# Kernel tuning notes

Measured on AMD Instinct MI355X. Metric: run time of the kernel, lower is better.

Reference implementation:

```python
import jax, jax.numpy as jnp
import numpy as np

N_ENSEMBLE = 50
STATE_DIM = 32
ACTION_DIM = 8
HIDDEN = 256
BATCH = 8192
OUT_DIM = STATE_DIM + 1  # next_state + reward


def setup_inputs() -> dict:
    key = jax.random.key(0)
    ks = jax.random.split(key, 8)
    s = 0.05  # small init scale to keep activations sane
    return {
        "state": jax.random.normal(ks[0], (BATCH, STATE_DIM), dtype=jnp.float32),
        "action": jax.random.normal(ks[1], (BATCH, ACTION_DIM), dtype=jnp.float32),
        "W1": jax.random.normal(ks[2], (N_ENSEMBLE, STATE_DIM + ACTION_DIM, HIDDEN), dtype=jnp.float32) * s,
        "b1": jnp.zeros((N_ENSEMBLE, HIDDEN), dtype=jnp.float32),
        "W2": jax.random.normal(ks[3], (N_ENSEMBLE, HIDDEN, HIDDEN), dtype=jnp.float32) * s,
        "b2": jnp.zeros((N_ENSEMBLE, HIDDEN), dtype=jnp.float32),
        "W3": jax.random.normal(ks[4], (N_ENSEMBLE, HIDDEN, HIDDEN), dtype=jnp.float32) * s,
        "b3": jnp.zeros((N_ENSEMBLE, HIDDEN), dtype=jnp.float32),
        "W4": jax.random.normal(ks[5], (N_ENSEMBLE, HIDDEN, OUT_DIM), dtype=jnp.float32) * s,
        "b4": jnp.zeros((N_ENSEMBLE, OUT_DIM), dtype=jnp.float32),
    }


def reference(state, action, W1, b1, W2, b2, W3, b3, W4, b4):
    # state_action: [B, S+A] shared across all ensemble members
    sa = jnp.concatenate((state, action), axis=1)
    # Batched-over-ensemble GEMMs replace the python loop over 50 MLPs.
    # h: [B, E, H]
    h = jax.nn.relu(jnp.einsum("bi,eih->beh", sa, W1) + b1)
    h = jax.nn.relu(jnp.einsum("beh,ehk->bek", h, W2) + b2)
    h = jax.nn.relu(jnp.einsum("beh,ehk->bek", h, W3) + b3)
    preds = jnp.einsum("beh,eho->beo", h, W4) + b4  # [B, E, S+1]
    return preds[..., :-1], preds[..., -1]
```

## Files before the change

### kernel.cpp

```cpp
#include <hip/hip_runtime.h>


typedef __attribute__((ext_vector_type(8))) short short8;
typedef __attribute__((ext_vector_type(4))) float floatx4;

#define NE 50
#define NB 8192
#define OUT_NS_ELEMS (NB * NE * 32)
#define OSTRIDE 48

__device__ __forceinline__ unsigned short f2bf_rne(float x) {
  unsigned u = __float_as_uint(x);
  u += 0x7fffu + ((u >> 16) & 1u);
  return (unsigned short)(u >> 16);
}
__device__ __forceinline__ float bf2f(unsigned short b) {
  return __uint_as_float(((unsigned)b) << 16);
}
__device__ __forceinline__ floatx4 mfma16(short8 a, short8 b, floatx4 c) {
  return __builtin_amdgcn_mfma_f32_16x16x32_bf16(a, b, c, 0, 0, 0);
}
__device__ __forceinline__ unsigned pack_bf2(float lo, float hi) {
  unsigned u0 = __float_as_uint(lo) + 0x8000u;
  unsigned u1 = __float_as_uint(hi) + 0x8000u;
  return __builtin_amdgcn_perm(u1, u0, 0x07060302u);
}

__device__ __forceinline__ unsigned short load_bf(const void* p, long i, bool isbf) {
  if (isbf) return ((const unsigned short*)p)[i];
  return f2bf_rne(((const float*)p)[i]);
}
__device__ __forceinline__ float load_f(const void* p, long i, bool isbf) {
  if (isbf) return bf2f(((const unsigned short*)p)[i]);
  return ((const float*)p)[i];
}

__device__ void pack_w_panel(const void* __restrict__ src, unsigned short* __restrict__ dst,
                             bool isbf, int e, int kt, int K, int N, int NT, int perE,
                             unsigned short* lds) {
  const int t = threadIdx.x;
  const int Npad = NT * 16;
  const int NP = Npad + 10;
  if (!isbf && N == Npad) {
    const int nq = Npad >> 2;
    for (int idx = t; idx < 32 * nq; idx += 256) {
      int r = idx / nq, q = idx - r * nq;
      int k = kt * 32 + r;
      unsigned short v0 = 0, v1 = 0, v2 = 0, v3 = 0;
      if (k < K) {
        const float4 f =
            *(const float4*)((const float*)src + ((long)(e * K + k) * N + q * 4));
        v0 = f2bf_rne(f.x); v1 = f2bf_rne(f.y);
        v2 = f2bf_rne(f.z); v3 = f2bf_rne(f.w);
      }
      unsigned* p = (unsigned*)(lds + r * NP + q * 4);
      p[0] = (unsigned)v0 | ((unsigned)v1 << 16);
      p[1] = (unsigned)v2 | ((unsigned)v3 << 16);
    }
  } else if (isbf && N == Npad) {
    const int no = Npad >> 3;
    for (int idx = t; idx < 32 * no; idx += 256) {
      int r = idx / no, q = idx - r * no;
      int k = kt * 32 + r;
      uint4 f = make_uint4(0u, 0u, 0u, 0u);
      if (k < K)
        f = *(const uint4*)((const unsigned short*)src + ((long)(e * K + k) * N + q * 8));
      unsigned* p = (unsigned*)(lds + r * NP + q * 8);
      p[0] = f.x; p[1] = f.y; p[2] = f.z; p[3] = f.w;
    }
  } else {
    for (int idx = t; idx < 32 * Npad; idx += 256) {
      int r = idx / Npad, c = idx - r * Npad;
      int k = kt * 32 + r;
      unsigned short v = 0;
      if (k < K && c < N) v = load_bf(src, (long)(e * K + k) * N + c, isbf);
      lds[r * NP + c] = v;
    }
  }
  __syncthreads();
  for (int u = t; u < NT * 64; u += 256) {
    int nt = u >> 6, kb = (u >> 4) & 3, ni = u & 15;
    int n = nt * 16 + ni;
    unsigned v[4];
#pragma unroll
    for (int p = 0; p < 4; ++p) {
      unsigned lo = lds[(kb * 8 + 2 * p) * NP + n];
      unsigned hi = lds[(kb * 8 + 2 * p + 1) * NP + n];
      v[p] = lo | (hi << 16);
    }
    long off = (long)e * perE + ((long)((kt * NT + nt) * 64 + kb * 16 + ni)) * 8;
    *(uint4*)(dst + off) = make_uint4(v[0], v[1], v[2], v[3]);
  }
}

__global__ void k_pack(const void* __restrict__ state, const void* __restrict__ action,
                       const void* __restrict__ W1, const void* __restrict__ W2,
                       const void* __restrict__ W3, const void* __restrict__ W4,
                       const void* __restrict__ b1, const void* __restrict__ b2,
                       const void* __restrict__ b3, const void* __restrict__ b4,
                       int isbfi,
                       unsigned short* __restrict__ saP, unsigned short* __restrict__ w1P,
                       unsigned short* __restrict__ w2P, unsigned short* __restrict__ w3P,
                       unsigned short* __restrict__ w4P, float* __restrict__ biasP) {
  __shared__ unsigned short lds[32 * 266];
  const bool isbf = (isbfi != 0);
  const int b = blockIdx.x;
  if (b < 400) {
    pack_w_panel(W2, w2P, isbf, b >> 3, b & 7, 256, 256, 16, 65536, lds);
  } else if (b < 800) {
    int bb = b - 400;
    pack_w_panel(W3, w3P, isbf, bb >> 3, bb & 7, 256, 256, 16, 65536, lds);
  } else if (b < 900) {
    int bb = b - 800;
    pack_w_panel(W1, w1P, isbf, bb >> 1, bb & 1, 40, 256, 16, 16384, lds);
  } else if (b < 1300) {
    int bb = b - 900;
    pack_w_panel(W4, w4P, isbf, bb >> 3, bb & 7, 256, 33, 3, 12288, lds);
  } else if (b < 1556) {
    int u = (b - 1300) * 256 + threadIdx.x;
    int mi = u & 15, kb = (u >> 4) & 7, mt = u >> 7;
    int row = mt * 16 + mi;
    unsigned v[4] = {0u, 0u, 0u, 0u};
    if (kb < 4) {
#pragma unroll
      for (int p = 0; p < 4; ++p) {
        unsigned lo = load_bf(state, (long)row * 32 + kb * 8 + 2 * p, isbf);
        unsigned hi = load_bf(state, (long)row * 32 + kb * 8 + 2 * p + 1, isbf);
        v[p] = lo | (hi << 16);
      }
    } else if (kb == 4) {
#pragma unroll
      for (int p = 0; p < 4; ++p) {
        unsigned lo = load_bf(action, (long)row * 8 + 2 * p, isbf);
        unsigned hi = load_bf(action, (long)row * 8 + 2 * p + 1, isbf);
        v[p] = lo | (hi << 16);
      }
    }
    *(uint4*)(saP + (long)u * 8) = make_uint4(v[0], v[1], v[2], v[3]);
  } else {
    int gid = (b - 1556) * 256 + threadIdx.x;
    if (gid < NE * 816) {
      int e = gid / 816, r = gid - e * 816;
      float v = 0.0f;
      if (r < 256)      v = load_f(b1, e * 256 + r,         isbf);
      else if (r < 512) v = load_f(b2, e * 256 + (r - 256), isbf);
      else if (r < 768) v = load_f(b3, e * 256 + (r - 512), isbf);
      else { int q = r - 768; if (q < 33) v = load_f(b4, e * 33 + q, isbf); }
      biasP[gid] = v;
    }
  }
}


__device__ __forceinline__ void store_tile16(const floatx4& a4, unsigned short* hT,
                                             int FT, int BT, int li, int g) {
  int k0 = FT * 16 + g * 4;
  unsigned d0 = pack_bf2(fmaxf(a4[0], 0.0f), fmaxf(a4[1], 0.0f));
  unsigned d1 = pack_bf2(fmaxf(a4[2], 0.0f), fmaxf(a4[3], 0.0f));
  int addr = ((k0 >> 5) * 4 + BT) * 512 + ((k0 >> 3) & 3) * 128 + li * 8 + (k0 & 7);
  *(unsigned long long*)(hT + addr) =
      (unsigned long long)d0 | ((unsigned long long)d1 << 32);
}

__device__ __forceinline__ void hidden_layer(const unsigned short* __restrict__ wp,
                                             const float* __restrict__ br,
                                             unsigned short* hT,
                                             int wf, int l, int li, int g) {
  floatx4 acc[4][4];
#pragma unroll
  for (int ot = 0; ot < 4; ++ot) {
    const float4 bq = *(const float4*)(br + wf * 64 + ot * 16 + g * 4);
    floatx4 iv = {bq.x, bq.y, bq.z, bq.w};
#pragma unroll
    for (int bt = 0; bt < 4; ++bt) acc[ot][bt] = iv;
  }
#pragma unroll
  for (int kt = 0; kt < 8; ++kt) {
    short8 a[4];
#pragma unroll
    for (int ot = 0; ot < 4; ++ot)
      a[ot] = *(const short8*)(wp + (long)((kt * 16 + wf * 4 + ot) * 64 + l) * 8);
#pragma unroll
    for (int bt = 0; bt < 4; ++bt) {
      short8 b = *(const short8*)(hT + ((kt * 4 + bt) * 64 + l) * 8);
#pragma unroll
      for (int ot = 0; ot < 4; ++ot)
        acc[ot][bt] = mfma16(a[ot], b, acc[ot][bt]);
    }
  }
  __syncthreads();
#pragma unroll
  for (int ot = 0; ot < 4; ++ot)
#pragma unroll
    for (int bt = 0; bt < 4; ++bt)
      store_tile16(acc[ot][bt], hT, wf * 4 + ot, bt, li, g);
  __syncthreads();
}

__global__ __launch_bounds__(256, 4) void k_mlp(
    const unsigned short* __restrict__ sa,
    const unsigned short* __restrict__ w1,
    const unsigned short* __restrict__ w2,
    const unsigned short* __restrict__ w3,
    const unsigned short* __restrict__ w4,
    const float* __restrict__ bias,
    int isbfi,
    float* __restrict__ rewardWS,
    void* __restrict__ outp) {
  __shared__ __attribute__((aligned(16))) unsigned short hT[16384];
  const int tid = threadIdx.x;
  const int wf = tid >> 6, l = tid & 63, li = l & 15, g = l >> 4;

  const int lid = blockIdx.y * 128 + blockIdx.x;
  const int swz = (lid & 7) * 800 + (lid >> 3);
  const int e  = swz >> 7;
  const int bb = swz & 127;

  const float* brow = bias + e * 816;
  const bool isbf = (isbfi != 0);

  {
    floatx4 acc[4][4];
#pragma unroll
    for (int ot = 0; ot < 4; ++ot) {
      const float4 bq = *(const float4*)(brow + wf * 64 + ot * 16 + g * 4);
      floatx4 iv = {bq.x, bq.y, bq.z, bq.w};
#pragma unroll
      for (int bt = 0; bt < 4; ++bt) acc[ot][bt] = iv;
    }
#pragma unroll
    for (int kt = 0; kt < 2; ++kt) {
      short8 a[4];
#pragma unroll
      for (int ot = 0; ot < 4; ++ot)
        a[ot] = *(const short8*)(w1 + (long)e * 16384 +
                                 (long)((kt * 16 + wf * 4 + ot) * 64 + l) * 8);
#pragma unroll
      for (int bt = 0; bt < 4; ++bt) {
        short8 b = *(const short8*)(sa + (long)((bb * 4 + bt) * 128 + kt * 64 + l) * 8);
#pragma unroll
        for (int ot = 0; ot < 4; ++ot)
          acc[ot][bt] = mfma16(a[ot], b, acc[ot][bt]);
      }
    }
#pragma unroll
    for (int ot = 0; ot < 4; ++ot)
#pragma unroll
      for (int bt = 0; bt < 4; ++bt)
        store_tile16(acc[ot][bt], hT, wf * 4 + ot, bt, li, g);
    __syncthreads();
  }

  hidden_layer(w2 + (long)e * 65536, brow + 256, hT, wf, l, li, g);
  hidden_layer(w3 + (long)e * 65536, brow + 512, hT, wf, l, li, g);

  const float* brow4 = brow + 768;
  floatx4 acc4[3];
#pragma unroll
  for (int ft = 0; ft < 3; ++ft) {
    const float4 bq = *(const float4*)(brow4 + ft * 16 + g * 4);
    floatx4 iv = {bq.x, bq.y, bq.z, bq.w};
    acc4[ft] = iv;
  }
#pragma unroll
  for (int kt = 0; kt < 8; ++kt) {
    short8 a[3];
#pragma unroll
    for (int ft = 0; ft < 3; ++ft)
      a[ft] = *(const short8*)(w4 + (long)e * 12288 + (long)((kt * 3 + ft) * 64 + l) * 8);
    short8 b = *(const short8*)(hT + ((kt * 4 + wf) * 64 + l) * 8);
#pragma unroll
    for (int ft = 0; ft < 3; ++ft)
      acc4[ft] = mfma16(a[ft], b, acc4[ft]);
  }

  if (g == 0) {
    rewardWS[(long)e * NB + bb * 64 + wf * 16 + li] = acc4[2][0];
  }

  __syncthreads();
#pragma unroll
  for (int ft = 0; ft < 2; ++ft) {
    int batch = wf * 16 + li;
    unsigned d0 = pack_bf2(acc4[ft][0], acc4[ft][1]);
    unsigned d1 = pack_bf2(acc4[ft][2], acc4[ft][3]);
    *(unsigned long long*)(hT + batch * OSTRIDE + ft * 16 + g * 4) =
        (unsigned long long)d0 | ((unsigned long long)d1 << 32);
  }
  __syncthreads();

  if (isbf) {
    unsigned short* o16 = (unsigned short*)outp;
    int batch = tid >> 2;
    int chunk = tid & 3;
    uint4 v = *(const uint4*)(hT + batch * OSTRIDE + chunk * 8);
    *(uint4*)(o16 + ((long)(bb * 64 + batch) * NE + e) * 32 + chunk * 8) = v;
  } else {
    float* o32 = (float*)outp;
#pragma unroll
    for (int p = 0; p < 2; ++p) {
      int idx = p * 256 + tid;
      int batch = idx >> 3;
      int chunk = idx & 7;
      const unsigned short* s = hT + batch * OSTRIDE + chunk * 4;
      *(float4*)(o32 + ((long)(bb * 64 + batch) * NE + e) * 32 + chunk * 4) =
          make_float4(bf2f(s[0]), bf2f(s[1]), bf2f(s[2]), bf2f(s[3]));
    }
  }
}

__global__ void k_reward(const float* __restrict__ rw, int isbfi,
                         void* __restrict__ outp) {
  int id = blockIdx.x * 256 + threadIdx.x;
  if (id >= NB * NE) return;
  int b = id / NE, e = id - b * NE;
  float v = rw[(long)e * NB + b];
  if (isbfi != 0) {
    unsigned u = __float_as_uint(v) + 0x8000u;
    ((unsigned short*)outp)[OUT_NS_ELEMS + id] = (unsigned short)(u >> 16);
  } else {
    ((float*)outp)[OUT_NS_ELEMS + id] = v;
  }
}

extern "C" void kernel_launch(void* const* d_in, const int* in_sizes, int n_in,
                              void* d_out, int out_size, void* d_ws, size_t ws_size,
                              hipStream_t stream) {
  const void* state  = d_in[0];
  const void* action = d_in[1];
  const void* W1 = d_in[2];
  const void* b1 = d_in[3];
  const void* W2 = d_in[4];
  const void* b2 = d_in[5];
  const void* W3 = d_in[6];
  const void* b3 = d_in[7];
  const void* W4 = d_in[8];
  const void* b4 = d_in[9];
  (void)n_in; (void)out_size; (void)ws_size;

  const int isbf = (in_sizes[4] == NE * 256 * 256 * 2) ? 1 : 0;

  char* ws = (char*)d_ws;
  unsigned short* saP    = (unsigned short*)(ws + 256);
  unsigned short* w1P    = (unsigned short*)(ws + 1048832);
  unsigned short* w2P    = (unsigned short*)(ws + 2687232);
  unsigned short* w3P    = (unsigned short*)(ws + 9240832);
  unsigned short* w4P    = (unsigned short*)(ws + 15794432);
  float* biasP           = (float*)(ws + 17023232);
  float* rewardWS        = (float*)(ws + 17186432);

  k_pack<<<1716, 256, 0, stream>>>(state, action, W1, W2, W3, W4, b1, b2, b3, b4,
                                   isbf, saP, w1P, w2P, w3P, w4P, biasP);
  k_mlp<<<dim3(128, 50), 256, 0, stream>>>(saP, w1P, w2P, w3P, w4P, biasP, isbf,
                                           rewardWS, d_out);
  k_reward<<<(NB * NE + 255) / 256, 256, 0, stream>>>(rewardWS, isbf, d_out);
}
```

Before: 236.3 us.

## Split weight packing into half-panels, vectorize input packing, add MFMA priority hints

Weight-panel packing now handles 16 K-rows per block instead of 32, which doubles the pack grid and halves the LDS staging buffer. This should raise occupancy and parallelism in the pack kernel. State/action packing now uses vectorized float4/uint4 loads, with each block handling four chunks instead of scalar loads. The MLP kernel wraps its MFMA inner loops in s_setprio(1)/s_setprio(0) so matrix issue gets priority over other waves. The extra blocks add launch overhead, and the setprio hints may have little effect.

```diff
diff --git a/kernel.cpp b/kernel.cpp
--- a/kernel.cpp
+++ b/kernel.cpp
@@ -35,17 +35,18 @@
   return ((const float*)p)[i];
 }
 
-__device__ void pack_w_panel(const void* __restrict__ src, unsigned short* __restrict__ dst,
-                             bool isbf, int e, int kt, int K, int N, int NT, int perE,
-                             unsigned short* lds) {
+__device__ void pack_w_panel16(const void* __restrict__ src, unsigned short* __restrict__ dst,
+                               bool isbf, int e, int kt, int h, int K, int N, int NT,
+                               int perE, unsigned short* lds) {
   const int t = threadIdx.x;
   const int Npad = NT * 16;
   const int NP = Npad + 10;
+  const int k0 = kt * 32 + h * 16;
   if (!isbf && N == Npad) {
     const int nq = Npad >> 2;
-    for (int idx = t; idx < 32 * nq; idx += 256) {
+    for (int idx = t; idx < 16 * nq; idx += 256) {
       int r = idx / nq, q = idx - r * nq;
-      int k = kt * 32 + r;
+      int k = k0 + r;
       unsigned short v0 = 0, v1 = 0, v2 = 0, v3 = 0;
       if (k < K) {
         const float4 f =
@@ -59,9 +60,9 @@
     }
   } else if (isbf && N == Npad) {
     const int no = Npad >> 3;
-    for (int idx = t; idx < 32 * no; idx += 256) {
+    for (int idx = t; idx < 16 * no; idx += 256) {
       int r = idx / no, q = idx - r * no;
-      int k = kt * 32 + r;
+      int k = k0 + r;
       uint4 f = make_uint4(0u, 0u, 0u, 0u);
       if (k < K)
         f = *(const uint4*)((const unsigned short*)src + ((long)(e * K + k) * N + q * 8));
@@ -69,23 +70,24 @@
       p[0] = f.x; p[1] = f.y; p[2] = f.z; p[3] = f.w;
     }
   } else {
-    for (int idx = t; idx < 32 * Npad; idx += 256) {
+    for (int idx = t; idx < 16 * Npad; idx += 256) {
       int r = idx / Npad, c = idx - r * Npad;
-      int k = kt * 32 + r;
+      int k = k0 + r;
       unsigned short v = 0;
       if (k < K && c < N) v = load_bf(src, (long)(e * K + k) * N + c, isbf);
       lds[r * NP + c] = v;
     }
   }
   __syncthreads();
-  for (int u = t; u < NT * 64; u += 256) {
-    int nt = u >> 6, kb = (u >> 4) & 3, ni = u & 15;
+  for (int u = t; u < NT * 32; u += 256) {
+    int ni = u & 15, kb_loc = (u >> 4) & 1, nt = u >> 5;
     int n = nt * 16 + ni;
+    int kb = 2 * h + kb_loc;
     unsigned v[4];
 #pragma unroll
     for (int p = 0; p < 4; ++p) {
-      unsigned lo = lds[(kb * 8 + 2 * p) * NP + n];
-      unsigned hi = lds[(kb * 8 + 2 * p + 1) * NP + n];
+      unsigned lo = lds[(kb_loc * 8 + 2 * p) * NP + n];
+      unsigned hi = lds[(kb_loc * 8 + 2 * p + 1) * NP + n];
       v[p] = lo | (hi << 16);
     }
     long off = (long)e * perE + ((long)((kt * NT + nt) * 64 + kb * 16 + ni)) * 8;
@@ -102,43 +104,56 @@
                        unsigned short* __restrict__ saP, unsigned short* __restrict__ w1P,
                        unsigned short* __restrict__ w2P, unsigned short* __restrict__ w3P,
                        unsigned short* __restrict__ w4P, float* __restrict__ biasP) {
-  __shared__ unsigned short lds[32 * 266];
+  __shared__ unsigned short lds[16 * 266];
   const bool isbf = (isbfi != 0);
   const int b = blockIdx.x;
-  if (b < 400) {
-    pack_w_panel(W2, w2P, isbf, b >> 3, b & 7, 256, 256, 16, 65536, lds);
-  } else if (b < 800) {
-    int bb = b - 400;
-    pack_w_panel(W3, w3P, isbf, bb >> 3, bb & 7, 256, 256, 16, 65536, lds);
-  } else if (b < 900) {
+  if (b < 800) {
+    pack_w_panel16(W2, w2P, isbf, b >> 4, (b & 15) >> 1, b & 1, 256, 256, 16, 65536, lds);
+  } else if (b < 1600) {
     int bb = b - 800;
-    pack_w_panel(W1, w1P, isbf, bb >> 1, bb & 1, 40, 256, 16, 16384, lds);
-  } else if (b < 1300) {
-    int bb = b - 900;
-    pack_w_panel(W4, w4P, isbf, bb >> 3, bb & 7, 256, 33, 3, 12288, lds);
-  } else if (b < 1556) {
-    int u = (b - 1300) * 256 + threadIdx.x;
-    int mi = u & 15, kb = (u >> 4) & 7, mt = u >> 7;
-    int row = mt * 16 + mi;
-    unsigned v[4] = {0u, 0u, 0u, 0u};
-    if (kb < 4) {
-#pragma unroll
-      for (int p = 0; p < 4; ++p) {
-        unsigned lo = load_bf(state, (long)row * 32 + kb * 8 + 2 * p, isbf);
-        unsigned hi = load_bf(state, (long)row * 32 + kb * 8 + 2 * p + 1, isbf);
-        v[p] = lo | (hi << 16);
+    pack_w_panel16(W3, w3P, isbf, bb >> 4, (bb & 15) >> 1, bb & 1, 256, 256, 16, 65536, lds);
+  } else if (b < 1800) {
+    int bb = b - 1600;
+    pack_w_panel16(W1, w1P, isbf, bb >> 2, (bb & 3) >> 1, bb & 1, 40, 256, 16, 16384, lds);
+  } else if (b < 2600) {
+    int bb = b - 1800;
+    pack_w_panel16(W4, w4P, isbf, bb >> 4, (bb & 15) >> 1, bb & 1, 256, 33, 3, 12288, lds);
+  } else if (b < 2664) {
+    int bb = b - 2600;
+#pragma unroll
+    for (int c = 0; c < 4; ++c) {
+      int u = bb * 1024 + c * 256 + threadIdx.x;
+      int mi = u & 15, kb = (u >> 4) & 7, mt = u >> 7;
+      int row = mt * 16 + mi;
+      uint4 v = make_uint4(0u, 0u, 0u, 0u);
+      if (isbf) {
+        if (kb < 4)
+          v = *(const uint4*)((const unsigned short*)state + (long)row * 32 + kb * 8);
+        else if (kb == 4)
+          v = *(const uint4*)((const unsigned short*)action + (long)row * 8);
+      } else {
+        if (kb < 4) {
+          const float* sp = (const float*)state + (long)row * 32 + kb * 8;
+          const float4 f0 = *(const float4*)(sp);
+          const float4 f1 = *(const float4*)(sp + 4);
+          v.x = (unsigned)f2bf_rne(f0.x) | ((unsigned)f2bf_rne(f0.y) << 16);
+          v.y = (unsigned)f2bf_rne(f0.z) | ((unsigned)f2bf_rne(f0.w) << 16);
+          v.z = (unsigned)f2bf_rne(f1.x) | ((unsigned)f2bf_rne(f1.y) << 16);
+          v.w = (unsigned)f2bf_rne(f1.z) | ((unsigned)f2bf_rne(f1.w) << 16);
+        } else if (kb == 4) {
+          const float* ap = (const float*)action + (long)row * 8;
+          const float4 f0 = *(const float4*)(ap);
+          const float4 f1 = *(const float4*)(ap + 4);
+          v.x = (unsigned)f2bf_rne(f0.x) | ((unsigned)f2bf_rne(f0.y) << 16);
+          v.y = (unsigned)f2bf_rne(f0.z) | ((unsigned)f2bf_rne(f0.w) << 16);
+          v.z = (unsigned)f2bf_rne(f1.x) | ((unsigned)f2bf_rne(f1.y) << 16);
+          v.w = (unsigned)f2bf_rne(f1.z) | ((unsigned)f2bf_rne(f1.w) << 16);
+        }
       }
-    } else if (kb == 4) {
-#pragma unroll
-      for (int p = 0; p < 4; ++p) {
-        unsigned lo = load_bf(action, (long)row * 8 + 2 * p, isbf);
-        unsigned hi = load_bf(action, (long)row * 8 + 2 * p + 1, isbf);
-        v[p] = lo | (hi << 16);
-      }
-    }
-    *(uint4*)(saP + (long)u * 8) = make_uint4(v[0], v[1], v[2], v[3]);
+      *(uint4*)(saP + (long)u * 8) = v;
+    }
   } else {
-    int gid = (b - 1556) * 256 + threadIdx.x;
+    int gid = (b - 2664) * 256 + threadIdx.x;
     if (gid < NE * 816) {
       int e = gid / 816, r = gid - e * 816;
       float v = 0.0f;
@@ -180,6 +195,7 @@
 #pragma unroll
     for (int ot = 0; ot < 4; ++ot)
       a[ot] = *(const short8*)(wp + (long)((kt * 16 + wf * 4 + ot) * 64 + l) * 8);
+    __builtin_amdgcn_s_setprio(1);
 #pragma unroll
     for (int bt = 0; bt < 4; ++bt) {
       short8 b = *(const short8*)(hT + ((kt * 4 + bt) * 64 + l) * 8);
@@ -187,6 +203,7 @@
       for (int ot = 0; ot < 4; ++ot)
         acc[ot][bt] = mfma16(a[ot], b, acc[ot][bt]);
     }
+    __builtin_amdgcn_s_setprio(0);
   }
   __syncthreads();
 #pragma unroll
@@ -235,6 +252,7 @@
       for (int ot = 0; ot < 4; ++ot)
         a[ot] = *(const short8*)(w1 + (long)e * 16384 +
                                  (long)((kt * 16 + wf * 4 + ot) * 64 + l) * 8);
+      __builtin_amdgcn_s_setprio(1);
 #pragma unroll
       for (int bt = 0; bt < 4; ++bt) {
         short8 b = *(const short8*)(sa + (long)((bb * 4 + bt) * 128 + kt * 64 + l) * 8);
@@ -242,6 +260,7 @@
         for (int ot = 0; ot < 4; ++ot)
           acc[ot][bt] = mfma16(a[ot], b, acc[ot][bt]);
       }
+      __builtin_amdgcn_s_setprio(0);
     }
 #pragma unroll
     for (int ot = 0; ot < 4; ++ot)
@@ -269,9 +288,11 @@
     for (int ft = 0; ft < 3; ++ft)
       a[ft] = *(const short8*)(w4 + (long)e * 12288 + (long)((kt * 3 + ft) * 64 + l) * 8);
     short8 b = *(const short8*)(hT + ((kt * 4 + wf) * 64 + l) * 8);
+    __builtin_amdgcn_s_setprio(1);
 #pragma unroll
     for (int ft = 0; ft < 3; ++ft)
       acc4[ft] = mfma16(a[ft], b, acc4[ft]);
+    __builtin_amdgcn_s_setprio(0);
   }
 
   if (g == 0) {
@@ -349,7 +370,7 @@
   float* biasP           = (float*)(ws + 17023232);
   float* rewardWS        = (float*)(ws + 17186432);
 
-  k_pack<<<1716, 256, 0, stream>>>(state, action, W1, W2, W3, W4, b1, b2, b3, b4,
+  k_pack<<<2824, 256, 0, stream>>>(state, action, W1, W2, W3, W4, b1, b2, b3, b4,
                                    isbf, saP, w1P, w2P, w3P, w4P, biasP);
   k_mlp<<<dim3(128, 50), 256, 0, stream>>>(saP, w1P, w2P, w3P, w4P, biasP, isbf,
                                            rewardWS, d_out);
```

Result: faster. 230.6 us (-2.4%).

## Vectorize input packing, add MFMA priority hints, LDS-transpose reward output

Applied to the files above, without the earlier changes.

The state/action packing now uses wide 16-byte loads with fp32 vector loads instead of per-element scalar loads, with each block handling four chunks. MFMA inner loops are wrapped in s_setprio raises so compute waves are favoured over load-issuing waves. The reward scatter kernel now transposes through shared memory so both the reads from the workspace and the writes to the output are coalesced, using 64 blocks. Block counts change to match, and the smaller reward grid may leave the GPU underused.

```diff
diff --git a/kernel.cpp b/kernel.cpp
--- a/kernel.cpp
+++ b/kernel.cpp
@@ -116,29 +116,42 @@
   } else if (b < 1300) {
     int bb = b - 900;
     pack_w_panel(W4, w4P, isbf, bb >> 3, bb & 7, 256, 33, 3, 12288, lds);
-  } else if (b < 1556) {
-    int u = (b - 1300) * 256 + threadIdx.x;
-    int mi = u & 15, kb = (u >> 4) & 7, mt = u >> 7;
-    int row = mt * 16 + mi;
-    unsigned v[4] = {0u, 0u, 0u, 0u};
-    if (kb < 4) {
-#pragma unroll
-      for (int p = 0; p < 4; ++p) {
-        unsigned lo = load_bf(state, (long)row * 32 + kb * 8 + 2 * p, isbf);
-        unsigned hi = load_bf(state, (long)row * 32 + kb * 8 + 2 * p + 1, isbf);
-        v[p] = lo | (hi << 16);
+  } else if (b < 1364) {
+    int bb = b - 1300;
+#pragma unroll
+    for (int c = 0; c < 4; ++c) {
+      int u = bb * 1024 + c * 256 + threadIdx.x;
+      int mi = u & 15, kb = (u >> 4) & 7, mt = u >> 7;
+      int row = mt * 16 + mi;
+      uint4 v = make_uint4(0u, 0u, 0u, 0u);
+      if (isbf) {
+        if (kb < 4)
+          v = *(const uint4*)((const unsigned short*)state + (long)row * 32 + kb * 8);
+        else if (kb == 4)
+          v = *(const uint4*)((const unsigned short*)action + (long)row * 8);
+      } else {
+        if (kb < 4) {
+          const float* sp = (const float*)state + (long)row * 32 + kb * 8;
+          const float4 f0 = *(const float4*)(sp);
+          const float4 f1 = *(const float4*)(sp + 4);
+          v.x = (unsigned)f2bf_rne(f0.x) | ((unsigned)f2bf_rne(f0.y) << 16);
+          v.y = (unsigned)f2bf_rne(f0.z) | ((unsigned)f2bf_rne(f0.w) << 16);
+          v.z = (unsigned)f2bf_rne(f1.x) | ((unsigned)f2bf_rne(f1.y) << 16);
+          v.w = (unsigned)f2bf_rne(f1.z) | ((unsigned)f2bf_rne(f1.w) << 16);
+        } else if (kb == 4) {
+          const float* ap = (const float*)action + (long)row * 8;
+          const float4 f0 = *(const float4*)(ap);
+          const float4 f1 = *(const float4*)(ap + 4);
+          v.x = (unsigned)f2bf_rne(f0.x) | ((unsigned)f2bf_rne(f0.y) << 16);
+          v.y = (unsigned)f2bf_rne(f0.z) | ((unsigned)f2bf_rne(f0.w) << 16);
+          v.z = (unsigned)f2bf_rne(f1.x) | ((unsigned)f2bf_rne(f1.y) << 16);
+          v.w = (unsigned)f2bf_rne(f1.z) | ((unsigned)f2bf_rne(f1.w) << 16);
+        }
       }
-    } else if (kb == 4) {
-#pragma unroll
-      for (int p = 0; p < 4; ++p) {
-        unsigned lo = load_bf(action, (long)row * 8 + 2 * p, isbf);
-        unsigned hi = load_bf(action, (long)row * 8 + 2 * p + 1, isbf);
-        v[p] = lo | (hi << 16);
-      }
-    }
-    *(uint4*)(saP + (long)u * 8) = make_uint4(v[0], v[1], v[2], v[3]);
+      *(uint4*)(saP + (long)u * 8) = v;
+    }
   } else {
-    int gid = (b - 1556) * 256 + threadIdx.x;
+    int gid = (b - 1364) * 256 + threadIdx.x;
     if (gid < NE * 816) {
       int e = gid / 816, r = gid - e * 816;
       float v = 0.0f;
@@ -180,6 +193,7 @@
 #pragma unroll
     for (int ot = 0; ot < 4; ++ot)
       a[ot] = *(const short8*)(wp + (long)((kt * 16 + wf * 4 + ot) * 64 + l) * 8);
+    __builtin_amdgcn_s_setprio(1);
 #pragma unroll
     for (int bt = 0; bt < 4; ++bt) {
       short8 b = *(const short8*)(hT + ((kt * 4 + bt) * 64 + l) * 8);
@@ -187,6 +201,7 @@
       for (int ot = 0; ot < 4; ++ot)
         acc[ot][bt] = mfma16(a[ot], b, acc[ot][bt]);
     }
+    __builtin_amdgcn_s_setprio(0);
   }
   __syncthreads();
 #pragma unroll
@@ -235,6 +250,7 @@
       for (int ot = 0; ot < 4; ++ot)
         a[ot] = *(const short8*)(w1 + (long)e * 16384 +
                                  (long)((kt * 16 + wf * 4 + ot) * 64 + l) * 8);
+      __builtin_amdgcn_s_setprio(1);
 #pragma unroll
       for (int bt = 0; bt < 4; ++bt) {
         short8 b = *(const short8*)(sa + (long)((bb * 4 + bt) * 128 + kt * 64 + l) * 8);
@@ -242,6 +258,7 @@
         for (int ot = 0; ot < 4; ++ot)
           acc[ot][bt] = mfma16(a[ot], b, acc[ot][bt]);
       }
+      __builtin_amdgcn_s_setprio(0);
     }
 #pragma unroll
     for (int ot = 0; ot < 4; ++ot)
@@ -269,9 +286,11 @@
     for (int ft = 0; ft < 3; ++ft)
       a[ft] = *(const short8*)(w4 + (long)e * 12288 + (long)((kt * 3 + ft) * 64 + l) * 8);
     short8 b = *(const short8*)(hT + ((kt * 4 + wf) * 64 + l) * 8);
+    __builtin_amdgcn_s_setprio(1);
 #pragma unroll
     for (int ft = 0; ft < 3; ++ft)
       acc4[ft] = mfma16(a[ft], b, acc4[ft]);
+    __builtin_amdgcn_s_setprio(0);
   }
 
   if (g == 0) {
@@ -311,15 +330,30 @@
 
 __global__ void k_reward(const float* __restrict__ rw, int isbfi,
                          void* __restrict__ outp) {
-  int id = blockIdx.x * 256 + threadIdx.x;
-  if (id >= NB * NE) return;
-  int b = id / NE, e = id - b * NE;
-  float v = rw[(long)e * NB + b];
+  __shared__ float lt[128 * 51];
+  const int t = threadIdx.x;
+  const int g = blockIdx.x;
+  for (int i = 0; i < 25; ++i) {
+    int idx = i * 256 + t;
+    int e = idx >> 7, bo = idx & 127;
+    lt[bo * 51 + e] = rw[(long)e * NB + g * 128 + bo];
+  }
+  __syncthreads();
   if (isbfi != 0) {
-    unsigned u = __float_as_uint(v) + 0x8000u;
-    ((unsigned short*)outp)[OUT_NS_ELEMS + id] = (unsigned short)(u >> 16);
+    unsigned short* o16 = (unsigned short*)outp + OUT_NS_ELEMS + g * 6400;
+    for (int i = 0; i < 25; ++i) {
+      int j = i * 256 + t;
+      int bo = j / 50, e = j - bo * 50;
+      unsigned u = __float_as_uint(lt[bo * 51 + e]) + 0x8000u;
+      o16[j] = (unsigned short)(u >> 16);
+    }
   } else {
-    ((float*)outp)[OUT_NS_ELEMS + id] = v;
+    float* o32 = (float*)outp + OUT_NS_ELEMS + g * 6400;
+    for (int i = 0; i < 25; ++i) {
+      int j = i * 256 + t;
+      int bo = j / 50, e = j - bo * 50;
+      o32[j] = lt[bo * 51 + e];
+    }
   }
 }
 
@@ -349,9 +383,9 @@
   float* biasP           = (float*)(ws + 17023232);
   float* rewardWS        = (float*)(ws + 17186432);
 
-  k_pack<<<1716, 256, 0, stream>>>(state, action, W1, W2, W3, W4, b1, b2, b3, b4,
+  k_pack<<<1524, 256, 0, stream>>>(state, action, W1, W2, W3, W4, b1, b2, b3, b4,
                                    isbf, saP, w1P, w2P, w3P, w4P, biasP);
   k_mlp<<<dim3(128, 50), 256, 0, stream>>>(saP, w1P, w2P, w3P, w4P, biasP, isbf,
                                            rewardWS, d_out);
-  k_reward<<<(NB * NE + 255) / 256, 256, 0, stream>>>(rewardWS, isbf, d_out);
-}
+  k_reward<<<64, 256, 0, stream>>>(rewardWS, isbf, d_out);
+}
```

After: 225.8 us. 1.05x faster.
